# Performance work log

Measured on AMD Instinct MI355X. Metric: run time of the kernel, lower is better.

The kernel has to match this reference:

```python
import jax, jax.numpy as jnp
import numpy as np

D_MODEL = 256; N_HEADS = 8; N_LEVELS = 4; N_POINTS = 4; NUM_ITER = 2
SHAPES = [(92, 160), (46, 80), (23, 40), (12, 20)]  # 4-level FPN, Len_in = 19560
LEN_IN = sum(h * w for h, w in SHAPES)
N_BATCH = 2


def _offset_bias():
    # faithful to _reset_parameters grid init of sampling_offsets.bias
    thetas = jnp.arange(N_HEADS, dtype=jnp.float32) * (2.0 * np.pi / N_HEADS)
    grid = jnp.stack([jnp.cos(thetas), jnp.sin(thetas)], -1)
    grid = grid / jnp.max(jnp.abs(grid), axis=-1, keepdims=True)
    grid = jnp.tile(grid[:, None, None, :], (1, N_LEVELS, N_POINTS, 1))
    grid = grid * (jnp.arange(N_POINTS, dtype=jnp.float32) + 1.0)[None, None, :, None]
    return grid.reshape(-1)


def setup_inputs() -> dict:
    key = jax.random.key(0)
    ks = jax.random.split(key, 12)
    N, Lq, d = N_BATCH, LEN_IN, D_MODEL
    s = 0.02
    return {
        "query0": jax.random.normal(ks[0], (N, Lq, d), jnp.float32),
        "query1": jax.random.normal(ks[1], (N, Lq, d), jnp.float32),
        "reference_points": jax.random.uniform(ks[2], (N, Lq, N_LEVELS, 2), jnp.float32),
        "input_flatten0": jax.random.normal(ks[3], (N, LEN_IN, d), jnp.float32),
        "input_flatten1": jax.random.normal(ks[4], (N, LEN_IN, d), jnp.float32),
        "input_spatial_shapes": jnp.array(SHAPES, jnp.int32),
        "input_level_start_index": jnp.array(np.cumsum([0] + [h * w for h, w in SHAPES[:-1]]), jnp.int32),
        "W_so": s * jax.random.normal(ks[5], (d, N_HEADS * N_LEVELS * N_POINTS * 2), jnp.float32),
        "b_so": _offset_bias(),
        "W_aw": s * jax.random.normal(ks[6], (d, N_HEADS * N_LEVELS * N_POINTS), jnp.float32),
        "b_aw": jnp.zeros((N_HEADS * N_LEVELS * N_POINTS,), jnp.float32),
        "W_v": s * jax.random.normal(ks[7], (d, d), jnp.float32),
        "b_v": jnp.zeros((d,), jnp.float32),
        "W_o": s * jax.random.normal(ks[8], (d, d), jnp.float32),
        "b_o": jnp.zeros((d,), jnp.float32),
        "W_agg": s * jax.random.normal(ks[9], (d * NUM_ITER, d), jnp.float32),
        "b_agg": jnp.zeros((d,), jnp.float32),
    }


def _sample_level(v_l, loc_l, H, W):
    # v_l: (N, nH, H*W, D); loc_l: (N, Lq, nH, P, 2) in [0,1]
    # bilinear, align_corners=False, zero padding (matches grid_sample fallback / CUDA kernel)
    x = loc_l[..., 0] * W - 0.5
    y = loc_l[..., 1] * H - 0.5
    x0 = jnp.floor(x); y0 = jnp.floor(y)

    def gather(xi, yi):
        inb = ((xi >= 0) & (xi <= W - 1) & (yi >= 0) & (yi <= H - 1)).astype(v_l.dtype)
        idx = (jnp.clip(yi, 0, H - 1) * W + jnp.clip(xi, 0, W - 1)).astype(jnp.int32)
        idx_t = jnp.transpose(idx, (0, 2, 1, 3))  # (N, nH, Lq, P)
        g = jax.vmap(jax.vmap(lambda vt, it: vt[it]))(v_l, idx_t)  # (N, nH, Lq, P, D)
        return g * jnp.transpose(inb, (0, 2, 1, 3))[..., None]

    def wt(w):
        return jnp.transpose(w, (0, 2, 1, 3))[..., None]

    return (wt((y0 + 1 - y) * (x0 + 1 - x)) * gather(x0, y0)
            + wt((y0 + 1 - y) * (x - x0)) * gather(x0 + 1, y0)
            + wt((y - y0) * (x0 + 1 - x)) * gather(x0, y0 + 1)
            + wt((y - y0) * (x - x0)) * gather(x0 + 1, y0 + 1))  # (N, nH, Lq, P, D)


def _ms_deform_attn(value, loc, attn, shapes, starts):
    # value: (N, Len_in, nH, D); loc: (N, Lq, nH, L, P, 2); attn: (N, Lq, nH, L, P)
    v = jnp.transpose(value, (0, 2, 1, 3))  # (N, nH, Len_in, D)
    acc = None
    for lvl in range(N_LEVELS):
        H, W = int(shapes[lvl, 0]), int(shapes[lvl, 1])
        s = int(starts[lvl])
        out_l = _sample_level(v[:, :, s:s + H * W], loc[:, :, :, lvl], H, W)
        a = jnp.transpose(attn[:, :, :, lvl], (0, 2, 1, 3))  # (N, nH, Lq, P)
        term = jnp.einsum('nhqpd,nhqp->nhqd', out_l, a)
        acc = term if acc is None else acc + term
    N, nH, Lq, D = acc.shape
    return jnp.transpose(acc, (0, 2, 1, 3)).reshape(N, Lq, nH * D)


def reference(query0, query1, reference_points, input_flatten0, input_flatten1,
              input_spatial_shapes, input_level_start_index,
              W_so, b_so, W_aw, b_aw, W_v, b_v, W_o, b_o, W_agg, b_agg):
    shapes = np.asarray(input_spatial_shapes)
    starts = np.asarray(input_level_start_index)
    N, Lq, d = query0.shape
    nH, L, P = N_HEADS, N_LEVELS, N_POINTS
    queries = [query0, query1]
    flats = [input_flatten0, input_flatten1]
    values, offs, aws = [], [], []
    for q, f in zip(queries, flats):
        values.append((f @ W_v + b_v).reshape(N, -1, nH, d // nH))
        offs.append((q @ W_so + b_so).reshape(N, Lq, nH, L, P, 2))
        aws.append((q @ W_aw + b_aw).reshape(N, Lq, nH, L * P))
    # joint softmax over num_iter * n_levels * n_points (the one-shot trick)
    aw_all = jax.nn.softmax(jnp.concatenate(aws, axis=-1), axis=-1)
    # (L, 2) normalizer = (W, H)
    normalizer = jnp.stack([input_spatial_shapes[..., 1], input_spatial_shapes[..., 0]], -1).astype(query0.dtype)
    outs = []
    for i in range(NUM_ITER):
        aw_i = aw_all[..., i * L * P:(i + 1) * L * P].reshape(N, Lq, nH, L, P)
        loc = reference_points[:, :, None, :, None, :] + offs[i] / normalizer[None, None, None, :, None, :]
        o = _ms_deform_attn(values[i], loc, aw_i, shapes, starts)
        outs.append(o @ W_o + b_o)
    return jnp.concatenate(outs, axis=-1) @ W_agg + b_agg
```

## Files before the change

kernel.cpp:

```cpp
#include <hip/hip_runtime.h>
#include <math.h>

#define NBATCH 2
#define LQ     19560
#define LEN    19560
#define NQ     (NBATCH * LQ)
#define DMODEL 256
#define NHEADS 8
#define HDIM   32
#define NLEV   4
#define NPTS   4
#define LDQS   384

typedef __bf16 bf16x8 __attribute__((ext_vector_type(8)));
typedef float  f32x4  __attribute__((ext_vector_type(4)));
typedef float  f32x2  __attribute__((ext_vector_type(2)));

__device__ inline float bf2f(unsigned short u) {
    return __uint_as_float(((unsigned int)u) << 16);
}
__device__ inline unsigned short f2bf(float f) {
    unsigned int u = __float_as_uint(f);
    u += 0x7FFFu + ((u >> 16) & 1u);
    return (unsigned short)(u >> 16);
}
__device__ inline f32x2 bfpair(unsigned int u) {
    f32x2 r;
    r.x = __uint_as_float(u << 16);
    r.y = __uint_as_float(u & 0xFFFF0000u);
    return r;
}

__global__ __launch_bounds__(256) void prep_all(
    const float* __restrict__ q0, const float* __restrict__ q1,
    const float* __restrict__ f0, const float* __restrict__ f1,
    const float* __restrict__ Wv, const float* __restrict__ Wso,
    const float* __restrict__ Waw, const float* __restrict__ bso,
    const float* __restrict__ baw,
    const float* __restrict__ Wo, const float* __restrict__ Wagg,
    const float* __restrict__ bo, const float* __restrict__ bagg,
    unsigned short* __restrict__ Qb0, unsigned short* __restrict__ Qb1,
    unsigned short* __restrict__ Fb0, unsigned short* __restrict__ Fb1,
    unsigned short* __restrict__ Wvt, unsigned short* __restrict__ Wsoawt,
    float* __restrict__ bsoaw,
    unsigned short* __restrict__ Wfcat, float* __restrict__ bfused)
{
    const int b = blockIdx.x;
    if (b < 19560) {
        const int tsel = b / 4890;
        const int x = b - tsel * 4890;
        const float* s = (tsel & 2) ? ((tsel & 1) ? f1 : f0) : ((tsel & 1) ? q1 : q0);
        unsigned short* d = (tsel & 2) ? ((tsel & 1) ? Fb1 : Fb0) : ((tsel & 1) ? Qb1 : Qb0);
        size_t i = ((size_t)x * 256 + threadIdx.x) * 8;
        float4 a = *(const float4*)(s + i);
        float4 c = *(const float4*)(s + i + 4);
        union { uint4 u; unsigned short h[8]; } t;
        t.h[0] = f2bf(a.x); t.h[1] = f2bf(a.y); t.h[2] = f2bf(a.z); t.h[3] = f2bf(a.w);
        t.h[4] = f2bf(c.x); t.h[5] = f2bf(c.y); t.h[6] = f2bf(c.z); t.h[7] = f2bf(c.w);
        *(uint4*)(d + i) = t.u;
    } else if (b < 19560 + 640) {
        int o = (b - 19560) * 256 + threadIdx.x;
        if (o < 65536) {
            int n = o >> 8, k = o & 255;
            Wvt[o] = f2bf(Wv[(size_t)k * 256 + n]);
        } else {
            int p = o - 65536;
            int n = p >> 8, k = p & 255;
            float v = (n < 256) ? Wso[(size_t)k * 256 + n] : Waw[(size_t)k * 128 + (n - 256)];
            Wsoawt[p] = f2bf(v);
        }
        if (o < 384) bsoaw[o] = (o < 256) ? bso[o] : baw[o - 256];
    } else {
        int k = b - 20200;
        int n = threadIdx.x;
        float s0 = 0.f, s1 = 0.f;
        for (int j = 0; j < 256; j++) {
            float w = Wo[k * 256 + j];
            s0 += w * Wagg[j * 256 + n];
            s1 += w * Wagg[(256 + j) * 256 + n];
        }
        Wfcat[(size_t)n * 512 + k]       = f2bf(s0);
        Wfcat[(size_t)n * 512 + 256 + k] = f2bf(s1);
        if (k == 0) {
            float bb = bagg[n];
            for (int j = 0; j < 256; j++)
                bb += bo[j] * (Wagg[j * 256 + n] + Wagg[(256 + j) * 256 + n]);
            bfused[n] = bb;
        }
    }
}

__global__ __launch_bounds__(256) void gemm_multi(
    const unsigned short* __restrict__ A0, const unsigned short* __restrict__ A1,
    const unsigned short* __restrict__ Bt, const float* __restrict__ bias,
    void* __restrict__ C0, void* __restrict__ C1,
    int M, int K, int lda, int N, int ldc, int mode)
{
    __shared__ __align__(16) unsigned short As[128 * 64];
    __shared__ __align__(16) unsigned short Bs[128 * 64];

    const int z = blockIdx.z;
    const unsigned short* A = z ? A1 : A0;
    void* Cv = z ? C1 : C0;

    const int tid  = threadIdx.x;
    const int w    = tid >> 6, lane = tid & 63;
    const int wm = w >> 1, wn = w & 1;
    const int m0 = blockIdx.y * 128, n0 = blockIdx.x * 128;
    const int lr = lane & 15, quad = lane >> 4;

    const int sr  = lane >> 3;
    const int scl = (lane & 7) ^ sr;
    const int colb = scl * 8;
    size_t arow[4], brow[4];
    #pragma unroll
    for (int j = 0; j < 4; j++) {
        int r = (w * 4 + j) * 8 + sr;
        int ra = m0 + r; if (ra > M - 1) ra = M - 1;
        arow[j] = (size_t)ra * lda;
        brow[j] = (size_t)(n0 + r) * K;
    }

    const f32x4 zero = {0.f, 0.f, 0.f, 0.f};
    f32x4 acc[4][4];
    #pragma unroll
    for (int i = 0; i < 4; i++)
        #pragma unroll
        for (int j = 0; j < 4; j++) acc[i][j] = zero;

    for (int t = 0; t < K; t += 64) {
        #pragma unroll
        for (int j = 0; j < 4; j++) {
            int lofs = __builtin_amdgcn_readfirstlane((w * 4 + j) * 1024);
            __builtin_amdgcn_global_load_lds(
                (const __attribute__((address_space(1))) void*)(A + arow[j] + t + colb),
                (__attribute__((address_space(3))) void*)((char*)As + lofs), 16, 0, 0);
            __builtin_amdgcn_global_load_lds(
                (const __attribute__((address_space(1))) void*)(Bt + brow[j] + t + colb),
                (__attribute__((address_space(3))) void*)((char*)Bs + lofs), 16, 0, 0);
        }
        __syncthreads();

        #pragma unroll
        for (int kk = 0; kk < 2; kk++) {
            bf16x8 af[4], bff[4];
            #pragma unroll
            for (int mi = 0; mi < 4; mi++) {
                int R = wm * 64 + mi * 16 + lr;
                int pc = ((kk * 4 + quad) ^ (lr & 7)) * 16;
                af[mi] = *(const bf16x8*)((const char*)As + R * 128 + pc);
            }
            #pragma unroll
            for (int ni = 0; ni < 4; ni++) {
                int R = wn * 64 + ni * 16 + lr;
                int pc = ((kk * 4 + quad) ^ (lr & 7)) * 16;
                bff[ni] = *(const bf16x8*)((const char*)Bs + R * 128 + pc);
            }
            #pragma unroll
            for (int mi = 0; mi < 4; mi++)
                #pragma unroll
                for (int ni = 0; ni < 4; ni++)
                    acc[mi][ni] = __builtin_amdgcn_mfma_f32_16x16x32_bf16(
                        af[mi], bff[ni], acc[mi][ni], 0, 0, 0);
        }
        __syncthreads();
    }

    float* Cf = (float*)Cv;
    unsigned short* Cb = (unsigned short*)Cv;
    #pragma unroll
    for (int mi = 0; mi < 4; mi++) {
        #pragma unroll
        for (int reg = 0; reg < 4; reg++) {
            int row = m0 + wm * 64 + mi * 16 + quad * 4 + reg;
            if (row >= M) continue;
            #pragma unroll
            for (int ni = 0; ni < 4; ni++) {
                int col = n0 + wn * 64 + ni * 16 + lr;
                float v = acc[mi][ni][reg];
                if (bias) v += bias[col];
                if (mode == 0) {
                    Cf[(size_t)row * ldc + col] = v;
                } else {
                    int n = row >= LQ ? 1 : 0;
                    int pos = row - n * LQ;
                    int h = col >> 5, d = col & 31;
                    Cb[((size_t)(n * NHEADS + h) * LEN + pos) * HDIM + d] = f2bf(v);
                }
            }
        }
    }
}

__global__ __launch_bounds__(256) void joint_softmax(float* __restrict__ QS0,
                                                     float* __restrict__ QS1)
{
    int r = blockIdx.x * 256 + threadIdx.x;
    if (r >= NQ * NHEADS) return;
    int nq = r >> 3, h = r & 7;
    float* p0 = QS0 + (size_t)nq * LDQS + 256 + h * 16;
    float* p1 = QS1 + (size_t)nq * LDQS + 256 + h * 16;
    float v[32];
    #pragma unroll
    for (int i = 0; i < 16; i++) { v[i] = p0[i]; v[16 + i] = p1[i]; }
    float m = v[0];
    #pragma unroll
    for (int i = 1; i < 32; i++) m = fmaxf(m, v[i]);
    float s = 0.f;
    #pragma unroll
    for (int i = 0; i < 32; i++) { v[i] = expf(v[i] - m); s += v[i]; }
    float inv = 1.0f / s;
    #pragma unroll
    for (int i = 0; i < 16; i++) { p0[i] = v[i] * inv; p1[i] = v[16 + i] * inv; }
}

#define QCHUNK 64
#define CHUNKS ((LQ + QCHUNK - 1) / QCHUNK)

__global__ __launch_bounds__(256) void ms_sample(
    const unsigned short* __restrict__ V0, const unsigned short* __restrict__ V1,
    const float* __restrict__ QS0, const float* __restrict__ QS1,
    const float* __restrict__ refp, unsigned short* __restrict__ Ocat)
{
    __shared__ unsigned short Sidx[16][64][4];
    __shared__ float          Swt [16][64][4];

    const int b = blockIdx.x;
    const int h = b & 7;
    const int rest = b >> 3;
    const int chunk = rest % CHUNKS;
    const int inn   = rest / CHUNKS;
    const int n  = inn & 1;
    const int it = inn >> 1;

    const int tid = threadIdx.x;
    const int ql  = tid >> 2;
    const int lj  = tid & 3;
    const int qraw = chunk * QCHUNK + ql;
    const bool valid = qraw < LQ;
    const int q  = valid ? qraw : LQ - 1;
    const int nq = n * LQ + q;

    const unsigned short* __restrict__ val = it ? V1 : V0;
    const float* __restrict__ QS = it ? QS1 : QS0;
    const unsigned short* __restrict__ vb2 =
        val + (size_t)(n * NHEADS + h) * LEN * HDIM;

    const int Hs[4] = {92, 46, 23, 12};
    const int Ws[4] = {160, 80, 40, 20};
    const int Ss[4] = {0, 14720, 18400, 19320};

    {
        const int H = Hs[lj], W = Ws[lj], S = Ss[lj];
        const float* prow = QS + (size_t)nq * LDQS;
        const float4 o0 = *(const float4*)(prow + (h << 5) + lj * 8);
        const float4 o1 = *(const float4*)(prow + (h << 5) + lj * 8 + 4);
        const float4 a4 = *(const float4*)(prow + 256 + (h << 4) + lj * 4);
        const float2 rp = *(const float2*)(refp + (size_t)nq * 8 + lj * 2);
        const float fx = rp.x * (float)W - 0.5f;
        const float fy = rp.y * (float)H - 0.5f;
        const float oxs[4] = {o0.x, o0.z, o1.x, o1.z};
        const float oys[4] = {o0.y, o0.w, o1.y, o1.w};
        const float avs[4] = {a4.x, a4.y, a4.z, a4.w};
        #pragma unroll
        for (int k = 0; k < NPTS; k++) {
            const float x = fx + oxs[k];
            const float y = fy + oys[k];
            const float x0f = floorf(x), y0f = floorf(y);
            const int x0 = (int)x0f, y0 = (int)y0f;
            const float wx1 = x - x0f, wy1 = y - y0f;
            const float wx0 = 1.0f - wx1, wy0 = 1.0f - wy1;
            const int xc0 = min(max(x0, 0), W - 1);
            const int xc1 = min(max(x0 + 1, 0), W - 1);
            const int yc0 = min(max(y0, 0), H - 1);
            const int yc1 = min(max(y0 + 1, 0), H - 1);
            const float a = avs[k];
            const float ay0 = ((unsigned int)y0 < (unsigned int)H) ? a * wy0 : 0.f;
            const float ay1 = ((unsigned int)(y0 + 1) < (unsigned int)H) ? a * wy1 : 0.f;
            const float mx0 = ((unsigned int)x0 < (unsigned int)W) ? wx0 : 0.f;
            const float mx1 = ((unsigned int)(x0 + 1) < (unsigned int)W) ? wx1 : 0.f;
            const int r0 = S + yc0 * W, r1 = S + yc1 * W;
            union { uint2 u; unsigned short s4[4]; } ip;
            ip.s4[0] = (unsigned short)(r0 + xc0);
            ip.s4[1] = (unsigned short)(r0 + xc1);
            ip.s4[2] = (unsigned short)(r1 + xc0);
            ip.s4[3] = (unsigned short)(r1 + xc1);
            *(uint2*)&Sidx[lj * 4 + k][ql][0] = ip.u;
            float4 w4 = make_float4(ay0 * mx0, ay0 * mx1, ay1 * mx0, ay1 * mx1);
            *(float4*)&Swt[lj * 4 + k][ql][0] = w4;
        }
    }
    __syncthreads();

    const int dl = lj << 3;
    const unsigned short* __restrict__ vdl = vb2 + dl;

    f32x2 acc[4];
    #pragma unroll
    for (int i = 0; i < 4; i++) acc[i] = (f32x2){0.f, 0.f};

    auto corner = [&](unsigned int eo, float wgt) {
        const uint4 c = *(const uint4*)(vdl + eo);
        const f32x2 w2 = {wgt, wgt};
        acc[0] += w2 * bfpair(c.x);
        acc[1] += w2 * bfpair(c.y);
        acc[2] += w2 * bfpair(c.z);
        acc[3] += w2 * bfpair(c.w);
    };

    #pragma unroll
    for (int p = 0; p < 16; p++) {
        const uint2 i2 = *(const uint2*)&Sidx[p][ql][0];
        const float4 w4 = *(const float4*)&Swt[p][ql][0];
        corner((i2.x & 0xFFFFu) << 5, w4.x);
        corner((i2.x >> 16) << 5, w4.y);
        corner((i2.y & 0xFFFFu) << 5, w4.z);
        corner((i2.y >> 16) << 5, w4.w);
    }

    if (valid) {
        union { uint4 u; unsigned short s[8]; } t;
        #pragma unroll
        for (int i = 0; i < 4; i++) {
            t.s[2 * i]     = f2bf(acc[i].x);
            t.s[2 * i + 1] = f2bf(acc[i].y);
        }
        *(uint4*)&Ocat[(size_t)nq * 512 + it * 256 + h * HDIM + dl] = t.u;
    }
}

extern "C" void kernel_launch(void* const* d_in, const int* in_sizes, int n_in,
                              void* d_out, int out_size, void* d_ws, size_t ws_size,
                              hipStream_t stream)
{
    const float* q0    = (const float*)d_in[0];
    const float* q1    = (const float*)d_in[1];
    const float* refp  = (const float*)d_in[2];
    const float* f0    = (const float*)d_in[3];
    const float* f1    = (const float*)d_in[4];
    const float* W_so  = (const float*)d_in[7];
    const float* b_so  = (const float*)d_in[8];
    const float* W_aw  = (const float*)d_in[9];
    const float* b_aw  = (const float*)d_in[10];
    const float* W_v   = (const float*)d_in[11];
    const float* b_v   = (const float*)d_in[12];
    const float* W_o   = (const float*)d_in[13];
    const float* b_o   = (const float*)d_in[14];
    const float* W_agg = (const float*)d_in[15];
    const float* b_agg = (const float*)d_in[16];
    float* out = (float*)d_out;

    float* ws = (float*)d_ws;
    float* QS0 = ws;
    float* QS1 = QS0 + (size_t)NQ * LDQS;
    unsigned short* V0   = (unsigned short*)(QS1 + (size_t)NQ * LDQS);
    unsigned short* V1   = V0 + (size_t)NQ * 256;
    unsigned short* Ocat = V1 + (size_t)NQ * 256;
    unsigned short* Wvt    = Ocat + (size_t)NQ * 512;
    unsigned short* Wsoawt = Wvt + 65536;
    unsigned short* Wfcat  = Wsoawt + 98304;
    float* bsoaw = (float*)(Wfcat + 131072);
    float* bfus  = bsoaw + 384;

    unsigned short* Qb0 = V0;
    unsigned short* Qb1 = V1;
    unsigned short* Fb0 = Ocat;
    unsigned short* Fb1 = Ocat + (size_t)NQ * 256;

    const int MB = (NQ + 127) / 128;
    dim3 blk(256);

    prep_all<<<20456, blk, 0, stream>>>(
        q0, q1, f0, f1, W_v, W_so, W_aw, b_so, b_aw, W_o, W_agg, b_o, b_agg,
        Qb0, Qb1, Fb0, Fb1, Wvt, Wsoawt, bsoaw, Wfcat, bfus);

    gemm_multi<<<dim3(3, MB, 2), blk, 0, stream>>>(
        Qb0, Qb1, Wsoawt, bsoaw, QS0, QS1, NQ, 256, 256, 384, LDQS, 0);

    joint_softmax<<<(NQ * NHEADS + 255) / 256, blk, 0, stream>>>(QS0, QS1);

    gemm_multi<<<dim3(2, MB, 2), blk, 0, stream>>>(
        Fb0, Fb1, Wvt, b_v, V0, V1, NQ, 256, 256, 256, 256, 2);

    ms_sample<<<2 * 2 * CHUNKS * 8, blk, 0, stream>>>(V0, V1, QS0, QS1, refp, Ocat);

    gemm_multi<<<dim3(2, MB, 1), blk, 0, stream>>>(
        Ocat, Ocat, Wfcat, bfus, out, out, NQ, 512, 512, 256, 256, 0);
}
```

Measured before the change: 542.1 us.

## Fuse joint softmax into attention-logit GEMM and split sampling setup into passes

The attention-weight logits GEMM for both iterations is moved into a dedicated kernel that computes both iterations' logits in one block and applies the joint softmax in registers via lane shuffles, removing the separate softmax kernel and its global round trip. The offset GEMM now covers only the first 256 columns. The sampling kernel computes its bilinear indices and weights in two passes of two levels each, with shared buffers halved and padded to 65 rows. This lowers shared-memory use and may reduce bank conflicts, at the cost of an extra barrier and more accumulator registers in the logits kernel.

Result: slower. 564.9 us (+4.2%).

```diff
diff --git a/kernel.cpp b/kernel.cpp
--- a/kernel.cpp
+++ b/kernel.cpp
@@ -192,26 +192,112 @@
     }
 }
 
-__global__ __launch_bounds__(256) void joint_softmax(float* __restrict__ QS0,
-                                                     float* __restrict__ QS1)
+__global__ __launch_bounds__(256) void gemm_logits(
+    const unsigned short* __restrict__ A0, const unsigned short* __restrict__ A1,
+    const unsigned short* __restrict__ Bt,
+    const float* __restrict__ bias,
+    float* __restrict__ C0, float* __restrict__ C1, int M)
 {
-    int r = blockIdx.x * 256 + threadIdx.x;
-    if (r >= NQ * NHEADS) return;
-    int nq = r >> 3, h = r & 7;
-    float* p0 = QS0 + (size_t)nq * LDQS + 256 + h * 16;
-    float* p1 = QS1 + (size_t)nq * LDQS + 256 + h * 16;
-    float v[32];
-    #pragma unroll
-    for (int i = 0; i < 16; i++) { v[i] = p0[i]; v[16 + i] = p1[i]; }
-    float m = v[0];
-    #pragma unroll
-    for (int i = 1; i < 32; i++) m = fmaxf(m, v[i]);
-    float s = 0.f;
-    #pragma unroll
-    for (int i = 0; i < 32; i++) { v[i] = expf(v[i] - m); s += v[i]; }
-    float inv = 1.0f / s;
-    #pragma unroll
-    for (int i = 0; i < 16; i++) { p0[i] = v[i] * inv; p1[i] = v[16 + i] * inv; }
+    __shared__ __align__(16) unsigned short As[128 * 64];
+    __shared__ __align__(16) unsigned short Bs[128 * 64];
+
+    const int tid  = threadIdx.x;
+    const int w    = tid >> 6, lane = tid & 63;
+    const int wm = w >> 1, wn = w & 1;
+    const int m0 = blockIdx.x * 128;
+    const int lr = lane & 15, quad = lane >> 4;
+
+    const int sr  = lane >> 3;
+    const int scl = (lane & 7) ^ sr;
+    const int colb = scl * 8;
+    size_t arow[4], brow[4];
+    #pragma unroll
+    for (int j = 0; j < 4; j++) {
+        int r = (w * 4 + j) * 8 + sr;
+        int ra = m0 + r; if (ra > M - 1) ra = M - 1;
+        arow[j] = (size_t)ra * 256;
+        brow[j] = (size_t)(256 + r) * 256;
+    }
+
+    const f32x4 zero = {0.f, 0.f, 0.f, 0.f};
+    f32x4 acc[2][4][4];
+    #pragma unroll
+    for (int zz = 0; zz < 2; zz++)
+        #pragma unroll
+        for (int i = 0; i < 4; i++)
+            #pragma unroll
+            for (int j = 0; j < 4; j++) acc[zz][i][j] = zero;
+
+    #pragma unroll
+    for (int z = 0; z < 2; z++) {
+        const unsigned short* A = z ? A1 : A0;
+        for (int t = 0; t < 256; t += 64) {
+            #pragma unroll
+            for (int j = 0; j < 4; j++) {
+                int lofs = __builtin_amdgcn_readfirstlane((w * 4 + j) * 1024);
+                __builtin_amdgcn_global_load_lds(
+                    (const __attribute__((address_space(1))) void*)(A + arow[j] + t + colb),
+                    (__attribute__((address_space(3))) void*)((char*)As + lofs), 16, 0, 0);
+                __builtin_amdgcn_global_load_lds(
+                    (const __attribute__((address_space(1))) void*)(Bt + brow[j] + t + colb),
+                    (__attribute__((address_space(3))) void*)((char*)Bs + lofs), 16, 0, 0);
+            }
+            __syncthreads();
+            #pragma unroll
+            for (int kk = 0; kk < 2; kk++) {
+                bf16x8 af[4], bff[4];
+                #pragma unroll
+                for (int mi = 0; mi < 4; mi++) {
+                    int R = wm * 64 + mi * 16 + lr;
+                    int pc = ((kk * 4 + quad) ^ (lr & 7)) * 16;
+                    af[mi] = *(const bf16x8*)((const char*)As + R * 128 + pc);
+                }
+                #pragma unroll
+                for (int ni = 0; ni < 4; ni++) {
+                    int R = wn * 64 + ni * 16 + lr;
+                    int pc = ((kk * 4 + quad) ^ (lr & 7)) * 16;
+                    bff[ni] = *(const bf16x8*)((const char*)Bs + R * 128 + pc);
+                }
+                #pragma unroll
+                for (int mi = 0; mi < 4; mi++)
+                    #pragma unroll
+                    for (int ni = 0; ni < 4; ni++)
+                        acc[z][mi][ni] = __builtin_amdgcn_mfma_f32_16x16x32_bf16(
+                            af[mi], bff[ni], acc[z][mi][ni], 0, 0, 0);
+            }
+            __syncthreads();
+        }
+    }
+
+    float bv[4];
+    #pragma unroll
+    for (int ni = 0; ni < 4; ni++) bv[ni] = bias[256 + wn * 64 + ni * 16 + lr];
+
+    #pragma unroll
+    for (int mi = 0; mi < 4; mi++) {
+        #pragma unroll
+        for (int reg = 0; reg < 4; reg++) {
+            int row = m0 + wm * 64 + mi * 16 + quad * 4 + reg;
+            #pragma unroll
+            for (int ni = 0; ni < 4; ni++) {
+                float a = acc[0][mi][ni][reg] + bv[ni];
+                float c = acc[1][mi][ni][reg] + bv[ni];
+                float m = fmaxf(a, c);
+                #pragma unroll
+                for (int d = 1; d < 16; d <<= 1) m = fmaxf(m, __shfl_xor(m, d));
+                float ea = expf(a - m), ec = expf(c - m);
+                float s = ea + ec;
+                #pragma unroll
+                for (int d = 1; d < 16; d <<= 1) s += __shfl_xor(s, d);
+                float inv = 1.0f / s;
+                if (row < M) {
+                    int col = 256 + wn * 64 + ni * 16 + lr;
+                    C0[(size_t)row * LDQS + col] = ea * inv;
+                    C1[(size_t)row * LDQS + col] = ec * inv;
+                }
+            }
+        }
+    }
 }
 
 #define QCHUNK 64
@@ -222,8 +308,8 @@
     const float* __restrict__ QS0, const float* __restrict__ QS1,
     const float* __restrict__ refp, unsigned short* __restrict__ Ocat)
 {
-    __shared__ unsigned short Sidx[16][64][4];
-    __shared__ float          Swt [16][64][4];
+    __shared__ unsigned short Sidx[8][65][4];
+    __shared__ float          Swt [8][65][4];
 
     const int b = blockIdx.x;
     const int h = b & 7;
@@ -250,48 +336,7 @@
     const int Ws[4] = {160, 80, 40, 20};
     const int Ss[4] = {0, 14720, 18400, 19320};
 
-    {
-        const int H = Hs[lj], W = Ws[lj], S = Ss[lj];
-        const float* prow = QS + (size_t)nq * LDQS;
-        const float4 o0 = *(const float4*)(prow + (h << 5) + lj * 8);
-        const float4 o1 = *(const float4*)(prow + (h << 5) + lj * 8 + 4);
-        const float4 a4 = *(const float4*)(prow + 256 + (h << 4) + lj * 4);
-        const float2 rp = *(const float2*)(refp + (size_t)nq * 8 + lj * 2);
-        const float fx = rp.x * (float)W - 0.5f;
-        const float fy = rp.y * (float)H - 0.5f;
-        const float oxs[4] = {o0.x, o0.z, o1.x, o1.z};
-        const float oys[4] = {o0.y, o0.w, o1.y, o1.w};
-        const float avs[4] = {a4.x, a4.y, a4.z, a4.w};
-        #pragma unroll
-        for (int k = 0; k < NPTS; k++) {
-            const float x = fx + oxs[k];
-            const float y = fy + oys[k];
-            const float x0f = floorf(x), y0f = floorf(y);
-            const int x0 = (int)x0f, y0 = (int)y0f;
-            const float wx1 = x - x0f, wy1 = y - y0f;
-            const float wx0 = 1.0f - wx1, wy0 = 1.0f - wy1;
-            const int xc0 = min(max(x0, 0), W - 1);
-            const int xc1 = min(max(x0 + 1, 0), W - 1);
-            const int yc0 = min(max(y0, 0), H - 1);
-            const int yc1 = min(max(y0 + 1, 0), H - 1);
-            const float a = avs[k];
-            const float ay0 = ((unsigned int)y0 < (unsigned int)H) ? a * wy0 : 0.f;
-            const float ay1 = ((unsigned int)(y0 + 1) < (unsigned int)H) ? a * wy1 : 0.f;
-            const float mx0 = ((unsigned int)x0 < (unsigned int)W) ? wx0 : 0.f;
-            const float mx1 = ((unsigned int)(x0 + 1) < (unsigned int)W) ? wx1 : 0.f;
-            const int r0 = S + yc0 * W, r1 = S + yc1 * W;
-            union { uint2 u; unsigned short s4[4]; } ip;
-            ip.s4[0] = (unsigned short)(r0 + xc0);
-            ip.s4[1] = (unsigned short)(r0 + xc1);
-            ip.s4[2] = (unsigned short)(r1 + xc0);
-            ip.s4[3] = (unsigned short)(r1 + xc1);
-            *(uint2*)&Sidx[lj * 4 + k][ql][0] = ip.u;
-            float4 w4 = make_float4(ay0 * mx0, ay0 * mx1, ay1 * mx0, ay1 * mx1);
-            *(float4*)&Swt[lj * 4 + k][ql][0] = w4;
-        }
-    }
-    __syncthreads();
-
+    const float* prow = QS + (size_t)nq * LDQS;
     const int dl = lj << 3;
     const unsigned short* __restrict__ vdl = vb2 + dl;
 
@@ -309,13 +354,61 @@
     };
 
     #pragma unroll
-    for (int p = 0; p < 16; p++) {
-        const uint2 i2 = *(const uint2*)&Sidx[p][ql][0];
-        const float4 w4 = *(const float4*)&Swt[p][ql][0];
-        corner((i2.x & 0xFFFFu) << 5, w4.x);
-        corner((i2.x >> 16) << 5, w4.y);
-        corner((i2.y & 0xFFFFu) << 5, w4.z);
-        corner((i2.y >> 16) << 5, w4.w);
+    for (int pass = 0; pass < 2; pass++) {
+        {
+            const int lvl = lj >> 1;
+            const int l   = (pass << 1) | lvl;
+            const int kb  = (lj & 1) << 1;
+            const int H = Hs[l], W = Ws[l], S = Ss[l];
+            const float2 rp = *(const float2*)(refp + (size_t)nq * 8 + l * 2);
+            const float fx = rp.x * (float)W - 0.5f;
+            const float fy = rp.y * (float)H - 0.5f;
+            const float4 off = *(const float4*)(prow + (h << 5) + l * 8 + (kb << 1));
+            const float2 aw2 = *(const float2*)(prow + 256 + (h << 4) + (l << 2) + kb);
+            const float oxs[2] = {off.x, off.z};
+            const float oys[2] = {off.y, off.w};
+            const float avs[2] = {aw2.x, aw2.y};
+            #pragma unroll
+            for (int i = 0; i < 2; i++) {
+                const float x = fx + oxs[i];
+                const float y = fy + oys[i];
+                const float x0f = floorf(x), y0f = floorf(y);
+                const int x0 = (int)x0f, y0 = (int)y0f;
+                const float wx1 = x - x0f, wy1 = y - y0f;
+                const float wx0 = 1.0f - wx1, wy0 = 1.0f - wy1;
+                const int xc0 = min(max(x0, 0), W - 1);
+                const int xc1 = min(max(x0 + 1, 0), W - 1);
+                const int yc0 = min(max(y0, 0), H - 1);
+                const int yc1 = min(max(y0 + 1, 0), H - 1);
+                const float a = avs[i];
+                const float ay0 = ((unsigned int)y0 < (unsigned int)H) ? a * wy0 : 0.f;
+                const float ay1 = ((unsigned int)(y0 + 1) < (unsigned int)H) ? a * wy1 : 0.f;
+                const float mx0 = ((unsigned int)x0 < (unsigned int)W) ? wx0 : 0.f;
+                const float mx1 = ((unsigned int)(x0 + 1) < (unsigned int)W) ? wx1 : 0.f;
+                const int r0 = S + yc0 * W, r1 = S + yc1 * W;
+                union { uint2 u; unsigned short s4[4]; } ip;
+                ip.s4[0] = (unsigned short)(r0 + xc0);
+                ip.s4[1] = (unsigned short)(r0 + xc1);
+                ip.s4[2] = (unsigned short)(r1 + xc0);
+                ip.s4[3] = (unsigned short)(r1 + xc1);
+                const int sp = (lvl << 2) + kb + i;
+                *(uint2*)&Sidx[sp][ql][0] = ip.u;
+                float4 w4 = make_float4(ay0 * mx0, ay0 * mx1, ay1 * mx0, ay1 * mx1);
+                *(float4*)&Swt[sp][ql][0] = w4;
+            }
+        }
+        __syncthreads();
+
+        #pragma unroll
+        for (int p = 0; p < 8; p++) {
+            const uint2 i2 = *(const uint2*)&Sidx[p][ql][0];
+            const float4 w4 = *(const float4*)&Swt[p][ql][0];
+            corner((i2.x & 0xFFFFu) << 5, w4.x);
+            corner((i2.x >> 16) << 5, w4.y);
+            corner((i2.y & 0xFFFFu) << 5, w4.z);
+            corner((i2.y >> 16) << 5, w4.w);
+        }
+        if (pass == 0) __syncthreads();
     }
 
     if (valid) {
@@ -374,10 +467,11 @@
         q0, q1, f0, f1, W_v, W_so, W_aw, b_so, b_aw, W_o, W_agg, b_o, b_agg,
         Qb0, Qb1, Fb0, Fb1, Wvt, Wsoawt, bsoaw, Wfcat, bfus);
 
-    gemm_multi<<<dim3(3, MB, 2), blk, 0, stream>>>(
+    gemm_multi<<<dim3(2, MB, 2), blk, 0, stream>>>(
         Qb0, Qb1, Wsoawt, bsoaw, QS0, QS1, NQ, 256, 256, 384, LDQS, 0);
 
-    joint_softmax<<<(NQ * NHEADS + 255) / 256, blk, 0, stream>>>(QS0, QS1);
+    gemm_logits<<<MB, blk, 0, stream>>>(
+        Qb0, Qb1, Wsoawt, bsoaw, QS0, QS1, NQ);
 
     gemm_multi<<<dim3(2, MB, 2), blk, 0, stream>>>(
         Fb0, Fb1, Wvt, b_v, V0, V1, NQ, 256, 256, 256, 256, 2);
```
